# Performance work log

Hardware: AMD Instinct MI355X
Metric: run time of the kernel (lower is better)

The kernel has to match this reference:

```python
import jax, jax.numpy as jnp
import numpy as np

SCALES = (128.0, 256.0, 512.0)
ASPECT = (0.5, 1.0, 2.0)
K = 9
NMS_THR = 0.7
PRE_NMS_TOPK = 10000
POST_NMS_TOPK = 2000
MIN_SIZE = 16.0

def conv2d(x, w, b, pad):
    out = jax.lax.conv_general_dilated(x, w, (1, 1), [(pad, pad), (pad, pad)], dimension_numbers=('NCHW', 'OIHW', 'NCHW'))
    return out + b[None, :, None, None]

def generate_anchors(grid_h, grid_w, dtype):
    # Faithful to source: shifts are grid indices, NOT multiplied by stride (source bug kept).
    scales = jnp.asarray(SCALES, dtype)
    ar = jnp.asarray(ASPECT, dtype)
    h_ratio = jnp.sqrt(ar)
    w_ratio = 1.0 / h_ratio
    ws = (w_ratio[:, None] * scales[None, :]).reshape(-1)
    hs = (h_ratio[:, None] * scales[None, :]).reshape(-1)
    base = jnp.round(jnp.stack([-ws, -hs, ws, hs], axis=1) / 2.0)  # (9,4)
    sy, sx = jnp.meshgrid(jnp.arange(grid_h), jnp.arange(grid_w), indexing='ij')
    sx = sx.reshape(-1).astype(dtype)
    sy = sy.reshape(-1).astype(dtype)
    shifts = jnp.stack([sx, sy, sx, sy], axis=1)  # (H*W,4)
    return (shifts[:, None, :] + base[None, :, :]).reshape(-1, 4)  # (H*W*9,4)

def decode(box_pred, anchors):
    w = anchors[:, 2] - anchors[:, 0]
    h = anchors[:, 3] - anchors[:, 1]
    cx = anchors[:, 0] + 0.5 * w
    cy = anchors[:, 1] + 0.5 * h
    dx, dy, dw, dh = box_pred[:, 0], box_pred[:, 1], box_pred[:, 2], box_pred[:, 3]
    pcx = dx * w + cx
    pcy = dy * h + cy
    pw = jnp.exp(dw) * w
    ph = jnp.exp(dh) * h
    return jnp.stack([pcx - 0.5 * pw, pcy - 0.5 * ph, pcx + 0.5 * pw, pcy + 0.5 * ph], axis=1)

def nms_keep(boxes, valid, thr):
    # Greedy NMS on score-descending boxes; invalid (small) boxes never kept nor suppress others.
    n = boxes.shape[0]
    x1, y1, x2, y2 = boxes[:, 0], boxes[:, 1], boxes[:, 2], boxes[:, 3]
    areas = (x2 - x1) * (y2 - y1)
    idx = jnp.arange(n)
    def body(i, keep):
        xx1 = jnp.maximum(x1, x1[i]); yy1 = jnp.maximum(y1, y1[i])
        xx2 = jnp.minimum(x2, x2[i]); yy2 = jnp.minimum(y2, y2[i])
        inter = jnp.maximum(xx2 - xx1, 0.0) * jnp.maximum(yy2 - yy1, 0.0)
        iou = inter / (areas + areas[i] - inter)
        suppress = (iou > thr) & (idx > i) & keep[i]
        return keep & (~suppress)
    return jax.lax.fori_loop(0, n, body, valid)

def filter_proposals(proposals, cls_scores, img_h, img_w):
    scores = jax.nn.sigmoid(cls_scores.reshape(-1))
    top_scores, top_idx = jax.lax.top_k(scores, PRE_NMS_TOPK)  # sorted descending
    props = proposals[top_idx]
    x1 = jnp.clip(props[:, 0], 0.0, img_w); y1 = jnp.clip(props[:, 1], 0.0, img_h)
    x2 = jnp.clip(props[:, 2], 0.0, img_w); y2 = jnp.clip(props[:, 3], 0.0, img_h)
    props = jnp.stack([x1, y1, x2, y2], axis=1)
    valid = ((x2 - x1) >= MIN_SIZE) & ((y2 - y1) >= MIN_SIZE)
    keep = jax.lax.stop_gradient(nms_keep(jax.lax.stop_gradient(props), valid, NMS_THR))
    masked = jnp.where(keep, top_scores, -1.0)
    final_scores, final_idx = jax.lax.top_k(masked, POST_NMS_TOPK)  # order = score-descending (matches post-NMS sort)
    final_props = props[final_idx]
    valid_out = final_scores > 0.0  # sigmoid scores > 0, padding = -1
    return jnp.where(valid_out[:, None], final_props, 0.0), jnp.where(valid_out, final_scores, 0.0)

def setup_inputs():
    key = jax.random.key(0)
    ks = jax.random.split(key, 8)
    C = 512; GH = GW = 50
    feat = jax.random.normal(ks[0], (1, C, GH, GW), jnp.float32)
    image = jnp.zeros((1, 3, 800, 800), jnp.float32)
    gt_boxes = jax.random.uniform(ks[1], (8, 4), jnp.float32) * 800.0
    w_rpn = jax.random.normal(ks[2], (C, C, 3, 3), jnp.float32) * 0.01
    b_rpn = jnp.zeros((C,), jnp.float32)
    w_cls = jax.random.normal(ks[3], (K, C, 1, 1), jnp.float32) * 0.01
    b_cls = jnp.zeros((K,), jnp.float32)
    w_reg = jax.random.normal(ks[4], (4 * K, C, 1, 1), jnp.float32) * 0.01
    b_reg = jnp.zeros((4 * K,), jnp.float32)
    return {"image": image, "feat": feat, "gt_boxes": gt_boxes, "w_rpn": w_rpn, "b_rpn": b_rpn, "w_cls": w_cls, "b_cls": b_cls, "w_reg": w_reg, "b_reg": b_reg}

def reference(image, feat, gt_boxes, w_rpn, b_rpn, w_cls, b_cls, w_reg, b_reg):
    rpn_feat = jax.nn.relu(conv2d(feat, w_rpn, b_rpn, 1))
    cls = conv2d(rpn_feat, w_cls, b_cls, 0)      # (B,9,H,W)
    reg = conv2d(rpn_feat, w_reg, b_reg, 0)      # (B,36,H,W)
    B, _, gh, gw = feat.shape
    anchors = generate_anchors(gh, gw, feat.dtype)
    # flatten to anchor ordering (h, w, k) matching generate_anchors
    cls_flat = jnp.transpose(cls, (0, 2, 3, 1)).reshape(-1)
    reg_flat = jnp.transpose(reg.reshape(B, K, 4, gh, gw), (0, 3, 4, 1, 2)).reshape(-1, 4)
    proposals = decode(reg_flat, anchors)
    img_h, img_w = float(image.shape[-2]), float(image.shape[-1])
    return filter_proposals(proposals, cls_flat, img_h, img_w)
```

## Files before the change

### kernel.cpp

```cpp
#include <hip/hip_runtime.h>
#include <cmath>
#include <cstdint>
#include <cstddef>

typedef unsigned long long u64;
typedef unsigned int u32;

#define NPX   2500
#define NANCH 22500
#define PRE_TOPK 10000
#define NWORDS 160

struct AnchorBase { float b[36]; };

typedef __attribute__((ext_vector_type(8))) short bf16x8;
typedef __attribute__((ext_vector_type(4))) float f32x4;

__device__ inline unsigned short f2bf(float f) {
    u32 u = __float_as_uint(f);
    u32 r = u + 0x7fffu + ((u >> 16) & 1u);
    return (unsigned short)(r >> 16);
}
__device__ inline float bf2f(unsigned short h) {
    return __uint_as_float(((u32)h) << 16);
}

__global__ __launch_bounds__(256) void kprep(const float* __restrict__ feat,
                                             const float* __restrict__ wr,
                                             unsigned short* __restrict__ xthi,
                                             unsigned short* __restrict__ xtlo,
                                             unsigned short* __restrict__ whi,
                                             unsigned short* __restrict__ wlo)
{
    __shared__ float sh[4608];
    int bid = blockIdx.x;
    int t = threadIdx.x;
    if (bid < 416) {
        float (*tile)[65] = (float(*)[65])sh;
        int gr = bid >> 3;
        int cc = bid & 7;
        int tx = t & 63, ty = t >> 6;
        int y = gr - 1;
        bool rowok = (gr >= 1) && (gr <= 50);
#pragma unroll
        for (int i = 0; i < 16; ++i) {
            int c = i * 4 + ty;
            tile[c][tx] = (rowok && tx < 50)
                        ? feat[(size_t)(cc * 64 + c) * NPX + y * 50 + tx] : 0.f;
        }
        __syncthreads();
#pragma unroll
        for (int i = 0; i < 16; ++i) {
            int xp = i * 4 + ty;
            int cell = gr * 64 + xp;
            bool ok = rowok && xp >= 1 && xp <= 50;
            float v = ok ? tile[tx][xp - 1] : 0.f;
            unsigned short hi = f2bf(v);
            xthi[(size_t)cell * 512 + cc * 64 + tx] = hi;
            xtlo[(size_t)cell * 512 + cc * 64 + tx] = f2bf(v - bf2f(hi));
        }
    } else {
        int oc = bid - 416;
        for (int j = t; j < 4608; j += 256) sh[j] = wr[(size_t)oc * 4608 + j];
        __syncthreads();
        for (int k = t; k < 4608; k += 256) {
            int c = k & 511, tap = k >> 9;
            float v = sh[c * 9 + tap];
            unsigned short hi = f2bf(v);
            whi[(size_t)oc * 4608 + k] = hi;
            wlo[(size_t)oc * 4608 + k] = f2bf(v - bf2f(hi));
        }
    }
}

__global__ __launch_bounds__(256) void k1m(const unsigned short* __restrict__ xthi,
                                           const unsigned short* __restrict__ xtlo,
                                           const unsigned short* __restrict__ whi,
                                           const unsigned short* __restrict__ wlo,
                                           float* __restrict__ pk,
                                           int cptLog, int cptm1, int cptMul, int niter)
{
    __shared__ __align__(16) unsigned short Ah[8192];
    __shared__ __align__(16) unsigned short Al[8192];
    __shared__ __align__(16) unsigned short Bh[4096];
    __shared__ __align__(16) unsigned short Bl[4096];

    int t = threadIdx.x;
    int lane = t & 63, wave = t >> 6;
    int wo = wave & 1, wp = wave >> 1;
    int ocb = blockIdx.x, pxb = blockIdx.y, bs = blockIdx.z;
    int q = lane >> 4, m = lane & 15;
    int c0base = bs * cptMul;

    int g  = t & 7;
    int r0 = t >> 3;
    int ocA[4];
    int cellB[2];
#pragma unroll
    for (int i = 0; i < 4; ++i) ocA[i] = ocb * 128 + r0 + 32 * i;
#pragma unroll
    for (int i = 0; i < 2; ++i) {
        int opx = pxb * 64 + r0 + 32 * i;
        cellB[i] = (opx < NPX) ? ((opx / 50) + 1) * 64 + (opx % 50) + 1 : 190;
    }

    f32x4 acc[8];
    f32x4 zf = {0.f, 0.f, 0.f, 0.f};
#pragma unroll
    for (int i = 0; i < 8; ++i) acc[i] = zf;

    for (int it = 0; it < niter; ++it) {
        int tap = it >> cptLog;
        int cw  = it & cptm1;
        int c0  = c0base + cw * 64;
        int t3  = (tap * 43) >> 7;
        int tapoff = (t3 - 1) * 64 + (tap - t3 * 3) - 1;
#pragma unroll
        for (int i = 0; i < 4; ++i) {
            int rl = r0 + 32 * i;
            int la = rl * 64 + g * 8;
            size_t ga = (size_t)ocA[i] * 4608 + tap * 512 + c0 + g * 8;
            *(bf16x8*)(Ah + la) = *(const bf16x8*)(whi + ga);
            *(bf16x8*)(Al + la) = *(const bf16x8*)(wlo + ga);
        }
#pragma unroll
        for (int i = 0; i < 2; ++i) {
            int rl = r0 + 32 * i;
            int la = rl * 64 + g * 8;
            size_t gb = (size_t)(cellB[i] + tapoff) * 512 + c0 + g * 8;
            *(bf16x8*)(Bh + la) = *(const bf16x8*)(xthi + gb);
            *(bf16x8*)(Bl + la) = *(const bf16x8*)(xtlo + gb);
        }
        __syncthreads();
#pragma unroll
        for (int ks = 0; ks < 2; ++ks) {
            bf16x8 fah[4], fal[4], fbh[2], fbl[2];
#pragma unroll
            for (int mt = 0; mt < 4; ++mt) {
                int off = (wo * 64 + mt * 16 + m) * 64 + ks * 32 + q * 8;
                fah[mt] = *(const bf16x8*)(Ah + off);
                fal[mt] = *(const bf16x8*)(Al + off);
            }
#pragma unroll
            for (int nt = 0; nt < 2; ++nt) {
                int off = (wp * 32 + nt * 16 + m) * 64 + ks * 32 + q * 8;
                fbh[nt] = *(const bf16x8*)(Bh + off);
                fbl[nt] = *(const bf16x8*)(Bl + off);
            }
#pragma unroll
            for (int mt = 0; mt < 4; ++mt)
#pragma unroll
                for (int nt = 0; nt < 2; ++nt) {
                    f32x4 a = acc[mt * 2 + nt];
                    a = __builtin_amdgcn_mfma_f32_16x16x32_bf16(fal[mt], fbh[nt], a, 0, 0, 0);
                    a = __builtin_amdgcn_mfma_f32_16x16x32_bf16(fah[mt], fbl[nt], a, 0, 0, 0);
                    a = __builtin_amdgcn_mfma_f32_16x16x32_bf16(fah[mt], fbh[nt], a, 0, 0, 0);
                    acc[mt * 2 + nt] = a;
                }
        }
        __syncthreads();
    }
#pragma unroll
    for (int mt = 0; mt < 4; ++mt)
#pragma unroll
        for (int nt = 0; nt < 2; ++nt)
#pragma unroll
            for (int r = 0; r < 4; ++r) {
                int oc = ocb * 128 + wo * 64 + mt * 16 + q * 4 + r;
                int px = pxb * 64 + wp * 32 + nt * 16 + m;
                pk[((size_t)bs * 512 + oc) * 2560 + px] = acc[mt * 2 + nt][r];
            }
}

__global__ __launch_bounds__(256) void k2a_heads(const float* __restrict__ pk, int ns,
                                                 const float* __restrict__ br,
                                                 const float* __restrict__ wcls,
                                                 const float* __restrict__ wreg,
                                                 float* __restrict__ part)
{
    __shared__ float vt[64 * 64];
    __shared__ float Wl[45 * 64];
    int t  = threadIdx.x;
    int pb = blockIdx.x;
    int s  = blockIdx.y;
    int cb = s * 64;
    for (int e = t; e < 45 * 64; e += 256) {
        int u = e >> 6, c = e & 63;
        Wl[e] = (u < 9) ? wcls[u * 512 + cb + c] : wreg[(u - 9) * 512 + cb + c];
    }
    int pxl = t & 63, ug = t >> 6;
    int px = pb * 64 + pxl;
    bool ok = px < NPX;
#pragma unroll
    for (int i = 0; i < 16; ++i) {
        int c = ug * 16 + i;
        float v = 0.f;
        if (ok) {
            size_t bidx = (size_t)(cb + c) * 2560 + px;
            v = br[cb + c];
            for (int ks = 0; ks < ns; ++ks) v += pk[(size_t)ks * 512 * 2560 + bidx];
            v = v > 0.f ? v : 0.f;
        }
        vt[c * 64 + pxl] = v;
    }
    __syncthreads();
    int ubase = ug * 12;
    int ulim  = (45 - ubase < 12) ? (45 - ubase) : 12;
    float acc[12];
#pragma unroll
    for (int j = 0; j < 12; ++j) acc[j] = 0.f;
    for (int c = 0; c < 64; ++c) {
        float v = vt[c * 64 + pxl];
#pragma unroll
        for (int j = 0; j < 12; ++j)
            acc[j] = fmaf(v, Wl[(ubase + j) * 64 + c], acc[j]);
    }
    if (ok) {
        for (int j = 0; j < ulim; ++j)
            part[((size_t)s * 45 + ubase + j) * NPX + px] = acc[j];
    }
}

__global__ __launch_bounds__(256) void k2b_decode(const float* __restrict__ part,
                                                  const float* __restrict__ bcls,
                                                  const float* __restrict__ breg,
                                                  AnchorBase ab,
                                                  float* __restrict__ score,
                                                  float* __restrict__ bx1, float* __restrict__ by1,
                                                  float* __restrict__ bx2, float* __restrict__ by2,
                                                  u32* __restrict__ valid,
                                                  u64* __restrict__ key)
{
    int id = blockIdx.x * 256 + threadIdx.x;
    if (id >= NANCH) return;
    int k  = id / NPX;
    int px = id - k * NPX;

    float z  = bcls[k];
    float d0 = breg[k * 4 + 0], d1 = breg[k * 4 + 1];
    float d2 = breg[k * 4 + 2], d3 = breg[k * 4 + 3];
#pragma unroll
    for (int s = 0; s < 8; ++s) {
        const float* p = part + (size_t)s * 45 * NPX;
        z  += p[(size_t)k * NPX + px];
        d0 += p[(size_t)(9 + k * 4 + 0) * NPX + px];
        d1 += p[(size_t)(9 + k * 4 + 1) * NPX + px];
        d2 += p[(size_t)(9 + k * 4 + 2) * NPX + px];
        d3 += p[(size_t)(9 + k * 4 + 3) * NPX + px];
    }
    float sc = 1.f / (1.f + expf(-z));

    int yy = px / 50, xx = px - (px / 50) * 50;
    float fx = (float)xx, fy = (float)yy;
    float ax1 = fx + ab.b[k * 4 + 0], ay1 = fy + ab.b[k * 4 + 1];
    float ax2 = fx + ab.b[k * 4 + 2], ay2 = fy + ab.b[k * 4 + 3];
    float aw = ax2 - ax1, ah = ay2 - ay1;
    float cx = ax1 + 0.5f * aw, cy = ay1 + 0.5f * ah;
    float pcx = d0 * aw + cx, pcy = d1 * ah + cy;
    float pw = expf(d2) * aw, ph = expf(d3) * ah;
    float x1 = pcx - 0.5f * pw, y1 = pcy - 0.5f * ph;
    float x2 = pcx + 0.5f * pw, y2 = pcy + 0.5f * ph;
    x1 = fminf(fmaxf(x1, 0.f), 800.f);
    y1 = fminf(fmaxf(y1, 0.f), 800.f);
    x2 = fminf(fmaxf(x2, 0.f), 800.f);
    y2 = fminf(fmaxf(y2, 0.f), 800.f);
    u32 v = ((x2 - x1) >= 16.f) && ((y2 - y1) >= 16.f);

    int f = px * 9 + k;
    score[f] = sc;
    bx1[f] = x1; by1[f] = y1; bx2[f] = x2; by2[f] = y2;
    valid[f] = v;
    u32 sb = __float_as_uint(sc);
    key[f] = ((u64)(~sb) << 32) | (u32)f;
}

__global__ __launch_bounds__(256) void k3a_rank(const u64* __restrict__ key,
                                                u32* __restrict__ rankp)
{
    __shared__ __align__(16) u64 sk[2250];
    int t  = threadIdx.x;
    int jb = blockIdx.y;
    for (int e = t; e < 2250; e += 256) sk[e] = key[jb * 2250 + e];
    __syncthreads();
    int i0 = blockIdx.x * 1024 + t;
    int i1 = i0 + 256, i2 = i0 + 512, i3 = i0 + 768;
    u64 k0 = (i0 < NANCH) ? key[i0] : 0ull;
    u64 k1 = (i1 < NANCH) ? key[i1] : 0ull;
    u64 k2 = (i2 < NANCH) ? key[i2] : 0ull;
    u64 k3 = (i3 < NANCH) ? key[i3] : 0ull;
    u32 c0 = 0, c1 = 0, c2 = 0, c3 = 0;
    const ulonglong2* sk2 = (const ulonglong2*)sk;
#pragma unroll 5
    for (int j = 0; j < 1125; ++j) {
        ulonglong2 v = sk2[j];
        c0 += (v.x < k0) ? 1u : 0u;  c0 += (v.y < k0) ? 1u : 0u;
        c1 += (v.x < k1) ? 1u : 0u;  c1 += (v.y < k1) ? 1u : 0u;
        c2 += (v.x < k2) ? 1u : 0u;  c2 += (v.y < k2) ? 1u : 0u;
        c3 += (v.x < k3) ? 1u : 0u;  c3 += (v.y < k3) ? 1u : 0u;
    }
    size_t base = (size_t)jb * NANCH;
    if (i0 < NANCH) rankp[base + i0] = c0;
    if (i1 < NANCH) rankp[base + i1] = c1;
    if (i2 < NANCH) rankp[base + i2] = c2;
    if (i3 < NANCH) rankp[base + i3] = c3;
}

__global__ __launch_bounds__(256) void k3b_gather(const u32* __restrict__ rankp,
                                                  const float* __restrict__ score,
                                                  const float* __restrict__ bx1, const float* __restrict__ by1,
                                                  const float* __restrict__ bx2, const float* __restrict__ by2,
                                                  const u32* __restrict__ valid,
                                                  float* __restrict__ sS,
                                                  float* __restrict__ sx1, float* __restrict__ sy1,
                                                  float* __restrict__ sx2, float* __restrict__ sy2,
                                                  float4* __restrict__ sbox4,
                                                  u32* __restrict__ sInv)
{
    int i = blockIdx.x * 256 + threadIdx.x;
    if (i >= NANCH) return;
    u32 r = 0;
#pragma unroll
    for (int c = 0; c < 10; ++c) r += rankp[(size_t)c * NANCH + i];
    if (r >= PRE_TOPK) return;
    float x1 = bx1[i], y1 = by1[i], x2 = bx2[i], y2 = by2[i];
    sS[r] = score[i];
    sx1[r] = x1; sy1[r] = y1; sx2[r] = x2; sy2[r] = y2;
    float4 b4; b4.x = x1; b4.y = y1; b4.z = x2; b4.w = y2;
    sbox4[r] = b4;
    sInv[r] = valid[i] ? 0u : 1u;
}

__global__ __launch_bounds__(256) void k4_mat(const float4* __restrict__ sbox4,
                                              u64* __restrict__ rows,
                                              u64* __restrict__ selfw)
{
    int t = threadIdx.x, lane = t & 63, wave = t >> 6;
    int i = blockIdx.x * 4 + wave;
    if (i >= PRE_TOPK) return;
    float4 bi = sbox4[i];
    float ai = (bi.z - bi.x) * (bi.w - bi.y);
    int wd  = i >> 6;
    int ish = i & 63;
    u64 diagmask = ~((2ull << ish) - 1ull);
    u64* rowp = rows + (size_t)i * NWORDS;
    for (int w = wd; w < 157; ++w) {
        float4 bj = sbox4[(w << 6) + lane];
        float xx1 = fmaxf(bi.x, bj.x);
        float yy1 = fmaxf(bi.y, bj.y);
        float xx2 = fminf(bi.z, bj.z);
        float yy2 = fminf(bi.w, bj.w);
        float iw = fmaxf(xx2 - xx1, 0.f);
        float ih = fmaxf(yy2 - yy1, 0.f);
        float inter = iw * ih;
        float aj = (bj.z - bj.x) * (bj.w - bj.y);
        float uni = ai + aj - inter;
        u64 b = __ballot(inter > 0.7f * uni);
        if (w == wd)  b &= diagmask;
        if (w == 156) b &= 0xFFFFull;
        if (lane == 0) {
            rowp[w] = b;
            if (w == wd) selfw[i] = b;
        }
    }
}

__global__ __launch_bounds__(64) void k5_scan(const u64* __restrict__ rows,
                                              const u64* __restrict__ selfw,
                                              const u32* __restrict__ sInv,
                                              const float* __restrict__ sS,
                                              const float* __restrict__ sx1, const float* __restrict__ sy1,
                                              const float* __restrict__ sx2, const float* __restrict__ sy2,
                                              float* __restrict__ out)
{
    __shared__ int keptList[2000];
    __shared__ int kcnt;
    int l = threadIdx.x;
    auto bw = [&](int w) -> u64 {
        const uint4* p = (const uint4*)(sInv + (size_t)w * 64);
        u64 v = 0;
#pragma unroll
        for (int j = 0; j < 16; ++j) {
            uint4 q = p[j];
            v |= ((u64)(q.x != 0) << (j * 4))     | ((u64)(q.y != 0) << (j * 4 + 1))
               | ((u64)(q.z != 0) << (j * 4 + 2)) | ((u64)(q.w != 0) << (j * 4 + 3));
        }
        return v;
    };
    u64 r0 = bw(l);
    u64 r1 = bw(64 + l);
    u64 r2 = (l < 32) ? bw(128 + l) : ~0ull;

    u64 cur[8], nxt[8];
#pragma unroll
    for (int k = 0; k < 8; ++k) cur[k] = selfw[(size_t)k * 64 + l];
#pragma unroll
    for (int k = 0; k < 8; ++k) {
        int ww = 8 + k;
        nxt[k] = (ww < 157) ? selfw[(size_t)ww * 64 + l] : 0ull;
    }

    int cnt = 0;
    bool done = false;
    for (int wg = 0; wg < 20; ++wg) {
#pragma unroll
        for (int ph = 0; ph < 8; ++ph) {
            int w = wg * 8 + ph;
            if (done || w > 156) continue;
            u64 swreg = cur[ph];
            int slot = w >> 6, owner = w & 63;
            u64 val = (slot == 0) ? r0 : (slot == 1) ? r1 : r2;
            u64 rw = __shfl(val, owner, 64);
            u64 wmask = (w == 156) ? 0xFFFFull : ~0ull;
            u64 av = (~rw) & wmask;
            u64 km = 0;
            while (av) {
                int b = __ffsll((unsigned long long)av) - 1;
                u64 sw = __shfl(swreg, b, 64);
                km |= 1ull << b;
                av &= ~(1ull << b);
                av &= ~sw;
            }
            u64 kk = km;
            while (kk) {
                int bsx[16];
                int nb = 0;
                while (kk && nb < 16) {
                    int b = __ffsll((unsigned long long)kk) - 1;
                    kk &= kk - 1;
                    bsx[nb++] = b;
                }
                u64 a0 = 0, a1 = 0, a2 = 0;
#pragma unroll
                for (int u = 0; u < 16; ++u) {
                    if (u < nb) {
                        int i = (w << 6) + bsx[u];
                        if (l == 0 && cnt + u < 2000) keptList[cnt + u] = i;
                        const u64* rp = rows + (size_t)i * NWORDS;
                        a0 |= rp[l];
                        a1 |= rp[64 + l];
                        if (l < 32) a2 |= rp[128 + l];
                    }
                }
                r0 |= a0; r1 |= a1; r2 |= a2;
                cnt += nb;
                if (cnt >= 2000) { done = true; break; }
            }
        }
        if (!done) {
            int base = (wg + 2) * 8;
#pragma unroll
            for (int k = 0; k < 8; ++k) cur[k] = nxt[k];
#pragma unroll
            for (int k = 0; k < 8; ++k) {
                int ww = base + k;
                nxt[k] = (ww < 157) ? selfw[(size_t)ww * 64 + l] : 0ull;
            }
        }
    }
    if (l == 0) kcnt = (cnt < 2000) ? cnt : 2000;
    __syncthreads();
    int K = kcnt;
    for (int r = l; r < 2000; r += 64) {
        if (r < K) {
            int j = keptList[r];
            out[r * 4 + 0] = sx1[j];
            out[r * 4 + 1] = sy1[j];
            out[r * 4 + 2] = sx2[j];
            out[r * 4 + 3] = sy2[j];
            out[8000 + r]  = sS[j];
        } else {
            out[r * 4 + 0] = 0.f; out[r * 4 + 1] = 0.f;
            out[r * 4 + 2] = 0.f; out[r * 4 + 3] = 0.f;
            out[8000 + r]  = 0.f;
        }
    }
}

extern "C" void kernel_launch(void* const* d_in, const int* in_sizes, int n_in,
                              void* d_out, int out_size, void* d_ws, size_t ws_size,
                              hipStream_t stream)
{
    (void)in_sizes; (void)n_in; (void)out_size;
    const float* feat = (const float*)d_in[1];
    const float* wrpn = (const float*)d_in[3];
    const float* brpn = (const float*)d_in[4];
    const float* wcls = (const float*)d_in[5];
    const float* bcls = (const float*)d_in[6];
    const float* wreg = (const float*)d_in[7];
    const float* breg = (const float*)d_in[8];
    float* out = (float*)d_out;

    int ns = (ws_size >= 58195968) ? 8 : (ws_size >= 37224448) ? 4 : 2;
    int cpt     = 8 / ns;
    int cptLog  = (ns == 2) ? 2 : (ns == 4) ? 1 : 0;
    int cptm1   = cpt - 1;
    int cptMul  = cpt * 64;
    int niter   = 9 * cpt;
    size_t pkB = (size_t)ns * 512 * 2560 * 4;

    char* ws = (char*)d_ws;
    float* pk = (float*)ws;
    unsigned short* Xthi = (unsigned short*)(ws + pkB);
    unsigned short* Xtlo = Xthi + (size_t)52 * 64 * 512;
    unsigned short* Whi  = (unsigned short*)(ws + pkB + 6815744);
    unsigned short* Wlo  = Whi + (size_t)512 * 4608;

    char* sm = ws + pkB;
    float* score = (float*)(sm + 0);
    float* bx1   = (float*)(sm + 90000);
    float* by1   = (float*)(sm + 180000);
    float* bx2   = (float*)(sm + 270000);
    float* by2   = (float*)(sm + 360000);
    u32*   valid = (u32*)  (sm + 450000);
    u64*   key   = (u64*)  (sm + 540000);
    u32*   rankp = (u32*)  (sm + 720000);
    float* sS    = (float*)(sm + 1620000);
    float* sx1   = (float*)(sm + 1660000);
    float* sy1   = (float*)(sm + 1700000);
    float* sx2   = (float*)(sm + 1740000);
    float* sy2   = (float*)(sm + 1780000);
    u32*   sInv  = (u32*)  (sm + 1820000);
    u64*   selfw = (u64*)  (sm + 1860960);
    float4* sbox4= (float4*)(sm + 1942880);
    float* part  = (float*)(sm + 2106720);
    u64*   rows  = (u64*)  (sm + 2106720);

    AnchorBase ab;
    {
        const float scales[3] = {128.f, 256.f, 512.f};
        const float aspect[3] = {0.5f, 1.f, 2.f};
        for (int ai = 0; ai < 3; ++ai) {
            float hr = sqrtf(aspect[ai]);
            float wratio = 1.0f / hr;
            for (int si = 0; si < 3; ++si) {
                float wsz = wratio * scales[si];
                float hsz = hr * scales[si];
                int a = ai * 3 + si;
                ab.b[a * 4 + 0] = rintf(-wsz / 2.0f);
                ab.b[a * 4 + 1] = rintf(-hsz / 2.0f);
                ab.b[a * 4 + 2] = rintf( wsz / 2.0f);
                ab.b[a * 4 + 3] = rintf( hsz / 2.0f);
            }
        }
    }

    kprep    <<<928, 256, 0, stream>>>(feat, wrpn, Xthi, Xtlo, Whi, Wlo);
    k1m      <<<dim3(4, 40, ns), 256, 0, stream>>>(Xthi, Xtlo, Whi, Wlo, pk,
                                                   cptLog, cptm1, cptMul, niter);
    k2a_heads<<<dim3(40, 8), 256, 0, stream>>>(pk, ns, brpn, wcls, wreg, part);
    k2b_decode<<<88, 256, 0, stream>>>(part, bcls, breg, ab, score, bx1, by1, bx2, by2, valid, key);
    k3a_rank <<<dim3(22, 10), 256, 0, stream>>>(key, rankp);
    k3b_gather<<<88, 256, 0, stream>>>(rankp, score, bx1, by1, bx2, by2, valid,
                                       sS, sx1, sy1, sx2, sy2, sbox4, sInv);
    hipMemsetAsync(rows, 0, (size_t)PRE_TOPK * NWORDS * 8, stream);
    k4_mat   <<<2500, 256, 0, stream>>>(sbox4, rows, selfw);
    k5_scan  <<<1, 64, 0, stream>>>(rows, selfw, sInv, sS, sx1, sy1, sx2, sy2, out);
}
```

Measured before the change: 371.7 us.

## Precompute unsuppressable NMS boxes in parallel, shrinking the serial scan's row loads

```diff
diff --git a/kernel.cpp b/kernel.cpp
--- a/kernel.cpp
+++ b/kernel.cpp
@@ -277,32 +277,39 @@
 __global__ __launch_bounds__(256) void k3a_rank(const u64* __restrict__ key,
                                                 u32* __restrict__ rankp)
 {
-    __shared__ __align__(16) u64 sk[2250];
+    __shared__ __align__(16) u64 sk[1126];
     int t  = threadIdx.x;
     int jb = blockIdx.y;
-    for (int e = t; e < 2250; e += 256) sk[e] = key[jb * 2250 + e];
+    for (int e = t; e < 1126; e += 256) {
+        int gj = jb * 1126 + e;
+        sk[e] = (gj < NANCH) ? key[gj] : ~0ull;
+    }
     __syncthreads();
-    int i0 = blockIdx.x * 1024 + t;
-    int i1 = i0 + 256, i2 = i0 + 512, i3 = i0 + 768;
-    u64 k0 = (i0 < NANCH) ? key[i0] : 0ull;
-    u64 k1 = (i1 < NANCH) ? key[i1] : 0ull;
-    u64 k2 = (i2 < NANCH) ? key[i2] : 0ull;
-    u64 k3 = (i3 < NANCH) ? key[i3] : 0ull;
-    u32 c0 = 0, c1 = 0, c2 = 0, c3 = 0;
+    int ib = blockIdx.x * 2048 + t;
+    u64 k0[8];
+    u32 cnt[8];
+#pragma unroll
+    for (int r = 0; r < 8; ++r) {
+        int i = ib + r * 256;
+        k0[r] = (i < NANCH) ? key[i] : 0ull;
+        cnt[r] = 0;
+    }
     const ulonglong2* sk2 = (const ulonglong2*)sk;
 #pragma unroll 5
-    for (int j = 0; j < 1125; ++j) {
+    for (int j = 0; j < 563; ++j) {
         ulonglong2 v = sk2[j];
-        c0 += (v.x < k0) ? 1u : 0u;  c0 += (v.y < k0) ? 1u : 0u;
-        c1 += (v.x < k1) ? 1u : 0u;  c1 += (v.y < k1) ? 1u : 0u;
-        c2 += (v.x < k2) ? 1u : 0u;  c2 += (v.y < k2) ? 1u : 0u;
-        c3 += (v.x < k3) ? 1u : 0u;  c3 += (v.y < k3) ? 1u : 0u;
+#pragma unroll
+        for (int r = 0; r < 8; ++r) {
+            cnt[r] += (v.x < k0[r]) ? 1u : 0u;
+            cnt[r] += (v.y < k0[r]) ? 1u : 0u;
+        }
     }
     size_t base = (size_t)jb * NANCH;
-    if (i0 < NANCH) rankp[base + i0] = c0;
-    if (i1 < NANCH) rankp[base + i1] = c1;
-    if (i2 < NANCH) rankp[base + i2] = c2;
-    if (i3 < NANCH) rankp[base + i3] = c3;
+#pragma unroll
+    for (int r = 0; r < 8; ++r) {
+        int i = ib + r * 256;
+        if (i < NANCH) rankp[base + i] = cnt[r];
+    }
 }
 
 __global__ __launch_bounds__(256) void k3b_gather(const u32* __restrict__ rankp,
@@ -320,7 +327,7 @@
     if (i >= NANCH) return;
     u32 r = 0;
 #pragma unroll
-    for (int c = 0; c < 10; ++c) r += rankp[(size_t)c * NANCH + i];
+    for (int c = 0; c < 20; ++c) r += rankp[(size_t)c * NANCH + i];
     if (r >= PRE_TOPK) return;
     float x1 = bx1[i], y1 = by1[i], x2 = bx2[i], y2 = by2[i];
     sS[r] = score[i];
@@ -335,60 +342,123 @@
                                               u64* __restrict__ selfw)
 {
     int t = threadIdx.x, lane = t & 63, wave = t >> 6;
-    int i = blockIdx.x * 4 + wave;
-    if (i >= PRE_TOPK) return;
-    float4 bi = sbox4[i];
-    float ai = (bi.z - bi.x) * (bi.w - bi.y);
-    int wd  = i >> 6;
-    int ish = i & 63;
-    u64 diagmask = ~((2ull << ish) - 1ull);
-    u64* rowp = rows + (size_t)i * NWORDS;
-    for (int w = wd; w < 157; ++w) {
+    int ig = (blockIdx.x * 4 + wave) * 4;
+    float4 bi[4];
+    float  ai[4];
+    int    wd[4];
+    u64    dm[4];
+#pragma unroll
+    for (int r = 0; r < 4; ++r) {
+        int i = ig + r;
+        bi[r] = sbox4[i];
+        ai[r] = (bi[r].z - bi[r].x) * (bi[r].w - bi[r].y);
+        wd[r] = i >> 6;
+        int ish = i & 63;
+        dm[r] = ~((2ull << ish) - 1ull);
+    }
+    for (int w = wd[0]; w < 157; ++w) {
         float4 bj = sbox4[(w << 6) + lane];
-        float xx1 = fmaxf(bi.x, bj.x);
-        float yy1 = fmaxf(bi.y, bj.y);
-        float xx2 = fminf(bi.z, bj.z);
-        float yy2 = fminf(bi.w, bj.w);
-        float iw = fmaxf(xx2 - xx1, 0.f);
-        float ih = fmaxf(yy2 - yy1, 0.f);
-        float inter = iw * ih;
         float aj = (bj.z - bj.x) * (bj.w - bj.y);
-        float uni = ai + aj - inter;
-        u64 b = __ballot(inter > 0.7f * uni);
-        if (w == wd)  b &= diagmask;
-        if (w == 156) b &= 0xFFFFull;
-        if (lane == 0) {
-            rowp[w] = b;
-            if (w == wd) selfw[i] = b;
-        }
-    }
-}
-
-__global__ __launch_bounds__(64) void k5_scan(const u64* __restrict__ rows,
-                                              const u64* __restrict__ selfw,
-                                              const u32* __restrict__ sInv,
-                                              const float* __restrict__ sS,
-                                              const float* __restrict__ sx1, const float* __restrict__ sy1,
-                                              const float* __restrict__ sx2, const float* __restrict__ sy2,
-                                              float* __restrict__ out)
+#pragma unroll
+        for (int r = 0; r < 4; ++r) {
+            if (w < wd[r]) continue;
+            float xx1 = fmaxf(bi[r].x, bj.x);
+            float yy1 = fmaxf(bi[r].y, bj.y);
+            float xx2 = fminf(bi[r].z, bj.z);
+            float yy2 = fminf(bi[r].w, bj.w);
+            float iw = fmaxf(xx2 - xx1, 0.f);
+            float ih = fmaxf(yy2 - yy1, 0.f);
+            float inter = iw * ih;
+            float uni = ai[r] + aj - inter;
+            u64 b = __ballot(inter > 0.7f * uni);
+            if (w == wd[r]) b &= dm[r];
+            if (w == 156)   b &= 0xFFFFull;
+            if (lane == 0) {
+                rows[(size_t)(ig + r) * NWORDS + w] = b;
+                if (w == wd[r]) selfw[ig + r] = b;
+            }
+        }
+    }
+}
+
+__global__ __launch_bounds__(256) void k5a_orall(const u64* __restrict__ rows,
+                                                 const u32* __restrict__ sInv,
+                                                 u64* __restrict__ remLow)
+{
+    int t = threadIdx.x, lane = t & 63, wave = t >> 6;
+    int wg = blockIdx.x * 4 + wave;
+    u64 a0 = 0, a1 = 0, a2 = 0;
+#pragma unroll
+    for (int rnd = 0; rnd < 2; ++rnd) {
+        int j0 = wg * 128 + rnd * 64;
+        int j  = j0 + lane;
+        u32 inv = (j < PRE_TOPK) ? sInv[j] : 1u;
+        u64 vm = __ballot(inv == 0u);
+        while (vm) {
+            int k = __ffsll((unsigned long long)vm) - 1;
+            vm &= vm - 1;
+            const u64* rp = rows + (size_t)(j0 + k) * NWORDS;
+            a0 |= rp[lane];
+            a1 |= rp[64 + lane];
+            if (lane < 32) a2 |= rp[128 + lane];
+        }
+    }
+    if (a0) atomicOr((unsigned long long*)(remLow + lane), (unsigned long long)a0);
+    if (a1) atomicOr((unsigned long long*)(remLow + 64 + lane), (unsigned long long)a1);
+    if (lane < 32 && a2) atomicOr((unsigned long long*)(remLow + 128 + lane), (unsigned long long)a2);
+}
+
+__global__ __launch_bounds__(256) void k5b_lower(const u64* __restrict__ rows,
+                                                 const u32* __restrict__ sInv,
+                                                 const u64* __restrict__ remLow,
+                                                 u64* __restrict__ remUp,
+                                                 u64* __restrict__ lowerBM)
+{
+    int t = threadIdx.x, lane = t & 63, wave = t >> 6;
+    int jw = blockIdx.x * 4 + wave;
+    int j  = jw * 64 + lane;
+    u32 inv = (j < PRE_TOPK) ? sInv[j] : 1u;
+    u64 rl = remLow[jw];
+    bool low = (inv == 0u) && !((rl >> lane) & 1ull);
+    u64 lowm = __ballot(low);
+    u64 invm = __ballot(inv != 0u);
+    if (lane == 0) {
+        if (lowm) atomicOr((unsigned long long*)(lowerBM + jw), (unsigned long long)lowm);
+        if (invm) atomicOr((unsigned long long*)(remUp + jw), (unsigned long long)invm);
+    }
+    u64 a0 = 0, a1 = 0, a2 = 0;
+    u64 vm = lowm;
+    while (vm) {
+        int k = __ffsll((unsigned long long)vm) - 1;
+        vm &= vm - 1;
+        const u64* rp = rows + (size_t)(jw * 64 + k) * NWORDS;
+        a0 |= rp[lane];
+        a1 |= rp[64 + lane];
+        if (lane < 32) a2 |= rp[128 + lane];
+    }
+    if (a0) atomicOr((unsigned long long*)(remUp + lane), (unsigned long long)a0);
+    if (a1) atomicOr((unsigned long long*)(remUp + 64 + lane), (unsigned long long)a1);
+    if (lane < 32 && a2) atomicOr((unsigned long long*)(remUp + 128 + lane), (unsigned long long)a2);
+}
+
+__global__ __launch_bounds__(64) void k5c_scan(const u64* __restrict__ rows,
+                                               const u64* __restrict__ selfw,
+                                               const u64* __restrict__ remUp,
+                                               const u64* __restrict__ lowerBM,
+                                               const float* __restrict__ sS,
+                                               const float* __restrict__ sx1, const float* __restrict__ sy1,
+                                               const float* __restrict__ sx2, const float* __restrict__ sy2,
+                                               float* __restrict__ out)
 {
     __shared__ int keptList[2000];
     __shared__ int kcnt;
     int l = threadIdx.x;
-    auto bw = [&](int w) -> u64 {
-        const uint4* p = (const uint4*)(sInv + (size_t)w * 64);
-        u64 v = 0;
-#pragma unroll
-        for (int j = 0; j < 16; ++j) {
-            uint4 q = p[j];
-            v |= ((u64)(q.x != 0) << (j * 4))     | ((u64)(q.y != 0) << (j * 4 + 1))
-               | ((u64)(q.z != 0) << (j * 4 + 2)) | ((u64)(q.w != 0) << (j * 4 + 3));
-        }
-        return v;
-    };
-    u64 r0 = bw(l);
-    u64 r1 = bw(64 + l);
-    u64 r2 = (l < 32) ? bw(128 + l) : ~0ull;
+    u64 r0 = remUp[l];
+    u64 r1 = remUp[64 + l];
+    u64 r2 = (l < 32) ? remUp[128 + l] : ~0ull;
+    u64 lb0 = lowerBM[l];
+    u64 lb1 = lowerBM[64 + l];
+    u64 lb2 = (l < 32) ? lowerBM[128 + l] : 0ull;
 
     u64 cur[8], nxt[8];
 #pragma unroll
@@ -408,19 +478,27 @@
             if (done || w > 156) continue;
             u64 swreg = cur[ph];
             int slot = w >> 6, owner = w & 63;
-            u64 val = (slot == 0) ? r0 : (slot == 1) ? r1 : r2;
-            u64 rw = __shfl(val, owner, 64);
+            u64 rv = (slot == 0) ? r0 : (slot == 1) ? r1 : r2;
+            u64 lv = (slot == 0) ? lb0 : (slot == 1) ? lb1 : lb2;
+            u64 rw = __shfl(rv, owner, 64);
+            u64 lw = __shfl(lv, owner, 64);
             u64 wmask = (w == 156) ? 0xFFFFull : ~0ull;
             u64 av = (~rw) & wmask;
-            u64 km = 0;
+            u64 loadset = 0;
             while (av) {
                 int b = __ffsll((unsigned long long)av) - 1;
-                u64 sw = __shfl(swreg, b, 64);
-                km |= 1ull << b;
-                av &= ~(1ull << b);
-                av &= ~sw;
-            }
-            u64 kk = km;
+                u64 bit = 1ull << b;
+                av &= ~bit;
+                if (l == 0) keptList[cnt] = (w << 6) + b;
+                cnt++;
+                if (cnt >= 2000) { done = true; break; }
+                if (!(lw & bit)) {
+                    loadset |= bit;
+                    u64 sw = __shfl(swreg, b, 64);
+                    av &= ~sw;
+                }
+            }
+            u64 kk = done ? 0ull : loadset;
             while (kk) {
                 int bsx[16];
                 int nb = 0;
@@ -434,7 +512,6 @@
                 for (int u = 0; u < 16; ++u) {
                     if (u < nb) {
                         int i = (w << 6) + bsx[u];
-                        if (l == 0 && cnt + u < 2000) keptList[cnt + u] = i;
                         const u64* rp = rows + (size_t)i * NWORDS;
                         a0 |= rp[l];
                         a1 |= rp[64 + l];
@@ -442,8 +519,6 @@
                     }
                 }
                 r0 |= a0; r1 |= a1; r2 |= a2;
-                cnt += nb;
-                if (cnt >= 2000) { done = true; break; }
             }
         }
         if (!done) {
@@ -514,16 +589,19 @@
     u32*   valid = (u32*)  (sm + 450000);
     u64*   key   = (u64*)  (sm + 540000);
     u32*   rankp = (u32*)  (sm + 720000);
-    float* sS    = (float*)(sm + 1620000);
-    float* sx1   = (float*)(sm + 1660000);
-    float* sy1   = (float*)(sm + 1700000);
-    float* sx2   = (float*)(sm + 1740000);
-    float* sy2   = (float*)(sm + 1780000);
-    u32*   sInv  = (u32*)  (sm + 1820000);
-    u64*   selfw = (u64*)  (sm + 1860960);
-    float4* sbox4= (float4*)(sm + 1942880);
-    float* part  = (float*)(sm + 2106720);
-    u64*   rows  = (u64*)  (sm + 2106720);
+    float* sS    = (float*)(sm + 2520000);
+    float* sx1   = (float*)(sm + 2560000);
+    float* sy1   = (float*)(sm + 2600000);
+    float* sx2   = (float*)(sm + 2640000);
+    float* sy2   = (float*)(sm + 2680000);
+    u32*   sInv  = (u32*)  (sm + 2720000);
+    u64*   selfw = (u64*)  (sm + 2760960);
+    float4* sbox4= (float4*)(sm + 2842880);
+    u64*   remLow= (u64*)  (sm + 3006720);
+    u64*   remUp = (u64*)  (sm + 3008000);
+    u64*   lowBM = (u64*)  (sm + 3009280);
+    float* part  = (float*)(sm + 3010560);
+    u64*   rows  = (u64*)  (sm + 3010560);
 
     AnchorBase ab;
     {
@@ -549,10 +627,14 @@
                                                    cptLog, cptm1, cptMul, niter);
     k2a_heads<<<dim3(40, 8), 256, 0, stream>>>(pk, ns, brpn, wcls, wreg, part);
     k2b_decode<<<88, 256, 0, stream>>>(part, bcls, breg, ab, score, bx1, by1, bx2, by2, valid, key);
-    k3a_rank <<<dim3(22, 10), 256, 0, stream>>>(key, rankp);
+    k3a_rank <<<dim3(11, 20), 256, 0, stream>>>(key, rankp);
     k3b_gather<<<88, 256, 0, stream>>>(rankp, score, bx1, by1, bx2, by2, valid,
                                        sS, sx1, sy1, sx2, sy2, sbox4, sInv);
     hipMemsetAsync(rows, 0, (size_t)PRE_TOPK * NWORDS * 8, stream);
-    k4_mat   <<<2500, 256, 0, stream>>>(sbox4, rows, selfw);
-    k5_scan  <<<1, 64, 0, stream>>>(rows, selfw, sInv, sS, sx1, sy1, sx2, sy2, out);
-}
+    hipMemsetAsync(remLow, 0, 3840, stream);
+    k4_mat   <<<625, 256, 0, stream>>>(sbox4, rows, selfw);
+    k5a_orall<<<20, 256, 0, stream>>>(rows, sInv, remLow);
+    k5b_lower<<<40, 256, 0, stream>>>(rows, sInv, remLow, remUp, lowBM);
+    k5c_scan <<<1, 64, 0, stream>>>(rows, selfw, remUp, lowBM,
+                                    sS, sx1, sy1, sx2, sy2, out);
+}
```

Measured after the change: 457.3 us. +23.0%, slower.
